# Optimization experiments

Hardware: AMD Instinct MI355X
Metric: run time of the kernel (lower is better)

Reference implementation:

```python
import jax, jax.numpy as jnp
import numpy as np

B, H, N = 2, 4, 4096


def setup_inputs() -> dict:
    key = jax.random.key(0)
    ranking = jax.random.normal(key, (B, H, N, 1), dtype=jnp.float32)
    return {"ranking": ranking}


def reference(ranking):
    b_s, h, n = ranking.shape[:3]
    r = ranking[..., 0]  # [b, h, n]
    # stable descending argsort of ranking*100 (negate; jnp stable sort keeps tie order)
    sorted_idx = jnp.argsort(-r * 100.0, axis=2, stable=True)  # [b, h, n] int
    r_sort = jnp.take_along_axis(r, sorted_idx, axis=2)
    # rel_scaler = cumsum of ones = 1..n (no mask case)
    rel_scaler = jnp.cumsum(jnp.ones_like(r_sort), axis=2)
    rel_minus = jnp.cumsum(r_sort, axis=2)
    relative_ranking = rel_minus - rel_scaler * r_sort
    rel_scaler = jnp.maximum(rel_scaler - 1.0, 0.0)  # 0..n-1
    # Hrelu forward: hard ReLU (custom backward in torch; forward math is relu)
    rank = jax.nn.relu(relative_ranking)
    indicator = rel_scaler - rank
    indicator = jnp.where(indicator < 0, indicator + n, indicator)
    perm_value = jnp.exp(-indicator * 10.0)
    # sparse COO (bh, row, col) -> coalesce == scatter-add into dense [b*h, n, n]
    rows = rel_scaler.astype(jnp.int32).reshape(b_s * h, n)
    cols = sorted_idx.reshape(b_s * h, n).astype(jnp.int32)
    vals = perm_value.reshape(b_s * h, n)
    bh = jnp.arange(b_s * h, dtype=jnp.int32)[:, None]
    perm = jnp.zeros((b_s * h, n, n), jnp.float32).at[bh, rows, cols].add(vals)
    return perm
```

## Files before the change

kernel.cpp:

```cpp
#include <hip/hip_runtime.h>
#include <math.h>

#define N 4096
#define BH 8
#define THREADS 256
#define PARTS 32
#define EPB 128
#define EPT 4
#define SLICES 8
#define KPS (N / SLICES)
#define CHUNK (N / THREADS)

__device__ __forceinline__ unsigned long long desc_key64(float r, int i) {
    float k = r * 100.0f;
    unsigned int b = __float_as_uint(k);
    unsigned int asc = (b & 0x80000000u) ? ~b : (b | 0x80000000u);
    return ((unsigned long long)(~asc) << 32) | (unsigned int)i;
}

__global__ __launch_bounds__(THREADS)
void rank_kernel(const float* __restrict__ ranking,
                 int* __restrict__ cols,
                 float* __restrict__ rsort) {
    __shared__ unsigned long long keys[N];
    __shared__ unsigned short partial[SLICES * EPB];

    const int bh   = blockIdx.x / PARTS;
    const int part = blockIdx.x % PARTS;
    const float* r = ranking + (size_t)bh * N;

    const float4* r4 = (const float4*)r;
    for (int i = threadIdx.x; i < N / 4; i += THREADS) {
        float4 w = r4[i];
        keys[i * 4 + 0] = desc_key64(w.x, i * 4 + 0);
        keys[i * 4 + 1] = desc_key64(w.y, i * 4 + 1);
        keys[i * 4 + 2] = desc_key64(w.z, i * 4 + 2);
        keys[i * 4 + 3] = desc_key64(w.w, i * 4 + 3);
    }
    __syncthreads();

    const int g = threadIdx.x & 31;
    const int s = threadIdx.x >> 5;
    const int e_base = g * EPT;

    unsigned long long mykey[EPT];
    #pragma unroll
    for (int j = 0; j < EPT; ++j)
        mykey[j] = keys[part * EPB + e_base + j];

    int cnt0 = 0, cnt1 = 0, cnt2 = 0, cnt3 = 0;
    const ulonglong2* k2 = (const ulonglong2*)(keys + s * KPS);
    #pragma unroll 4
    for (int k = 0; k < KPS / 2; ++k) {
        ulonglong2 kk = k2[k];
        cnt0 += (kk.x < mykey[0]) + (kk.y < mykey[0]);
        cnt1 += (kk.x < mykey[1]) + (kk.y < mykey[1]);
        cnt2 += (kk.x < mykey[2]) + (kk.y < mykey[2]);
        cnt3 += (kk.x < mykey[3]) + (kk.y < mykey[3]);
    }
    partial[s * EPB + e_base + 0] = (unsigned short)cnt0;
    partial[s * EPB + e_base + 1] = (unsigned short)cnt1;
    partial[s * EPB + e_base + 2] = (unsigned short)cnt2;
    partial[s * EPB + e_base + 3] = (unsigned short)cnt3;
    __syncthreads();

    if (threadIdx.x < EPB) {
        int rank = 0;
        #pragma unroll
        for (int t = 0; t < SLICES; ++t)
            rank += (int)partial[t * EPB + threadIdx.x];
        int e = part * EPB + threadIdx.x;
        size_t o = (size_t)bh * N + rank;
        cols[o]  = e;
        rsort[o] = r[e];
    }
}

__global__ __launch_bounds__(THREADS)
void scanscatter_kernel(const int* __restrict__ cols,
                        const float* __restrict__ rsort,
                        float* __restrict__ out) {
    __shared__ double sdata[THREADS];

    const int tid  = threadIdx.x;
    const int bh   = blockIdx.x;
    const int base = tid * CHUNK;

    int c[CHUNK];
    const int4* c4 = (const int4*)(cols + (size_t)bh * N + base);
    #pragma unroll
    for (int q = 0; q < CHUNK / 4; ++q) {
        int4 w = c4[q];
        c[q * 4 + 0] = w.x; c[q * 4 + 1] = w.y;
        c[q * 4 + 2] = w.z; c[q * 4 + 3] = w.w;
    }

    const float* rs = rsort + (size_t)bh * N;
    float  v[CHUNK];
    double local[CHUNK];
    const float4* f4 = (const float4*)(rs + base);
    #pragma unroll
    for (int q = 0; q < CHUNK / 4; ++q) {
        float4 w = f4[q];
        v[q * 4 + 0] = w.x; v[q * 4 + 1] = w.y;
        v[q * 4 + 2] = w.z; v[q * 4 + 3] = w.w;
    }
    double ssum = 0.0;
    #pragma unroll
    for (int q = 0; q < CHUNK; ++q) { ssum += (double)v[q]; local[q] = ssum; }

    sdata[tid] = ssum;
    __syncthreads();
    #pragma unroll
    for (int s = 1; s < THREADS; s <<= 1) {
        double y = (tid >= s) ? sdata[tid - s] : 0.0;
        __syncthreads();
        sdata[tid] += y;
        __syncthreads();
    }
    const double off = sdata[tid] - ssum;

    float* obase = out + (size_t)bh * N * N;
    #pragma unroll
    for (int q = 0; q < CHUNK; ++q) {
        int i = base + q;
        double cumsum = off + local[q];
        double rel    = cumsum - (double)(i + 1) * (double)v[q];
        double rank   = rel > 0.0 ? rel : 0.0;
        double ind    = (double)i - rank;
        if (ind < 0.0) ind += (double)N;
        if (ind < 0.0) ind = 0.0;
        obase[(size_t)i * N + c[q]] = (float)exp(ind * -10.0);
    }
}

extern "C" void kernel_launch(void* const* d_in, const int* in_sizes, int n_in,
                              void* d_out, int out_size, void* d_ws, size_t ws_size,
                              hipStream_t stream) {
    const float* ranking = (const float*)d_in[0];
    float* out = (float*)d_out;

    int*   cols  = (int*)d_ws;
    float* rsort = (float*)((char*)d_ws + sizeof(int) * (size_t)BH * N);

    rank_kernel<<<BH * PARTS, THREADS, 0, stream>>>(ranking, cols, rsort);

    hipMemsetAsync(out, 0, sizeof(float) * (size_t)BH * N * N, stream);

    scanscatter_kernel<<<BH, THREADS, 0, stream>>>(cols, rsort, out);
}
```

Baseline: 532.5 us.

## Fuse zero-fill and scatter into one dense write pass over output

Replaces the hipMemsetAsync plus the scattered single-element writes with a kernel that writes every output row once, using 16-byte vector stores. Each row is zeros except for its one permutation value, which is injected in place. The scan now writes per-row values to workspace first, and a third kernel then streams the whole 512 MB output. This removes the separate memset pass and its launch, at the cost of an extra small kernel and workspace traffic.

```diff
diff --git a/kernel.cpp b/kernel.cpp
--- a/kernel.cpp
+++ b/kernel.cpp
@@ -10,6 +10,10 @@
 #define SLICES 8
 #define KPS (N / SLICES)
 #define CHUNK (N / THREADS)
+#define FB 256
+#define RPF (BH * N / FB)
+
+typedef float f32x4 __attribute__((ext_vector_type(4)));
 
 __device__ __forceinline__ unsigned long long desc_key64(float r, int i) {
     float k = r * 100.0f;
@@ -77,23 +81,13 @@
 }
 
 __global__ __launch_bounds__(THREADS)
-void scanscatter_kernel(const int* __restrict__ cols,
-                        const float* __restrict__ rsort,
-                        float* __restrict__ out) {
+void scanvals_kernel(const float* __restrict__ rsort,
+                     float* __restrict__ vals) {
     __shared__ double sdata[THREADS];
 
     const int tid  = threadIdx.x;
     const int bh   = blockIdx.x;
     const int base = tid * CHUNK;
-
-    int c[CHUNK];
-    const int4* c4 = (const int4*)(cols + (size_t)bh * N + base);
-    #pragma unroll
-    for (int q = 0; q < CHUNK / 4; ++q) {
-        int4 w = c4[q];
-        c[q * 4 + 0] = w.x; c[q * 4 + 1] = w.y;
-        c[q * 4 + 2] = w.z; c[q * 4 + 3] = w.w;
-    }
 
     const float* rs = rsort + (size_t)bh * N;
     float  v[CHUNK];
@@ -120,7 +114,7 @@
     }
     const double off = sdata[tid] - ssum;
 
-    float* obase = out + (size_t)bh * N * N;
+    float* vo = vals + (size_t)bh * N;
     #pragma unroll
     for (int q = 0; q < CHUNK; ++q) {
         int i = base + q;
@@ -130,7 +124,41 @@
         double ind    = (double)i - rank;
         if (ind < 0.0) ind += (double)N;
         if (ind < 0.0) ind = 0.0;
-        obase[(size_t)i * N + c[q]] = (float)exp(ind * -10.0);
+        vo[i] = (float)exp(ind * -10.0);
+    }
+}
+
+__global__ __launch_bounds__(THREADS)
+void fillinject_kernel(const int* __restrict__ cols,
+                       const float* __restrict__ vals,
+                       float* __restrict__ out) {
+    __shared__ int   sc[RPF];
+    __shared__ float sv[RPF];
+
+    const int tid = threadIdx.x;
+    const size_t g0 = (size_t)blockIdx.x * RPF;
+
+    for (int i = tid; i < RPF; i += THREADS) {
+        sc[i] = cols[g0 + i];
+        sv[i] = vals[g0 + i];
+    }
+    __syncthreads();
+
+    f32x4* o = (f32x4*)(out + g0 * N);
+    #pragma unroll 1
+    for (int kk = 0; kk < (RPF * (N / 4)) / THREADS; kk += 4) {
+        const int   row  = kk >> 2;
+        const int   c    = sc[row];
+        const float v    = sv[row];
+        const int   fc   = c >> 2;
+        const int   lane = c & 3;
+        #pragma unroll
+        for (int q = 0; q < 4; ++q) {
+            int idx_in_row = (q << 8) | tid;
+            f32x4 w = {0.f, 0.f, 0.f, 0.f};
+            if (idx_in_row == fc) w[lane] = v;
+            o[(size_t)(kk + q) * THREADS + tid] = w;
+        }
     }
 }
 
@@ -142,10 +170,9 @@
 
     int*   cols  = (int*)d_ws;
     float* rsort = (float*)((char*)d_ws + sizeof(int) * (size_t)BH * N);
+    float* vals  = (float*)((char*)d_ws + (sizeof(int) + sizeof(float)) * (size_t)BH * N);
 
     rank_kernel<<<BH * PARTS, THREADS, 0, stream>>>(ranking, cols, rsort);
-
-    hipMemsetAsync(out, 0, sizeof(float) * (size_t)BH * N * N, stream);
-
-    scanscatter_kernel<<<BH, THREADS, 0, stream>>>(cols, rsort, out);
+    scanvals_kernel<<<BH, THREADS, 0, stream>>>(rsort, vals);
+    fillinject_kernel<<<FB, THREADS, 0, stream>>>(cols, vals, out);
 }
```

New measurement: 530.0 us. About the same (-0.5%).
